# Kernel tuning notes

Measured on AMD Instinct MI355X. Metric: run time of the kernel, lower is better.

The kernel has to match this reference:

```python
import jax, jax.numpy as jnp
import numpy as np

B, L, D, H, P = 8, 1024, 128, 128, 8
W = 2 * L  # total words
FT = 0.1   # forget-gate floor


def _lin_init(k, out_d, in_d):
    k1, k2 = jax.random.split(k)
    s = 1.0 / np.sqrt(in_d)
    Wm = jax.random.uniform(k1, (out_d, in_d), minval=-s, maxval=s, dtype=jnp.float32)
    b = jax.random.uniform(k2, (out_d,), minval=-s, maxval=s, dtype=jnp.float32)
    return Wm, b


def setup_inputs() -> dict:
    key = jax.random.key(0)
    ks = jax.random.split(key, 32)
    inp = {
        "word_span0": jax.random.normal(ks[0], (B, L, D), dtype=jnp.float32),
        "word_span1": jax.random.normal(ks[1], (B, L, D), dtype=jnp.float32),
        "node_hidden": jax.random.normal(ks[2], (B, D), dtype=jnp.float32),
        "op_embedding": jax.random.normal(ks[3], (B, P, D), dtype=jnp.float32),
        "word_exist_sequence": jax.random.uniform(ks[4], (B, W), dtype=jnp.float32),
        "word_exist_matrix": jax.random.uniform(ks[5], (B, W, W), dtype=jnp.float32),
        "word_operator": jax.random.uniform(ks[6], (B, W, P), dtype=jnp.float32),
        "word_word": jax.random.uniform(ks[7], (B, W, W), dtype=jnp.float32),
        "depend0": jax.random.uniform(ks[8], (B, L, L), dtype=jnp.float32),
        "depend1": jax.random.uniform(ks[9], (B, L, L), dtype=jnp.float32),
        "goal_word": jax.random.uniform(ks[10], (B, W), dtype=jnp.float32),
    }
    dims = [("w_w_s", H, D), ("w_w_k", H, D), ("w_update", D, 3 * H),
            ("g_w", H, D), ("w_o", D, D), ("b2u_forget", D, 3 * H + D),
            ("b2u_forget2", D, 2 * D), ("linear_output", D, D),
            ("o_w", H, D), ("w_g", D, D), ("u2b_forget", D, 2 * D),
            ("w_o_forget", P, D + P * D), ("w_o_rel", P, D + P * D),
            ("w_o_update", P, 2 * P)]
    for i, (nm, o, ii) in enumerate(dims):
        Wm, b = _lin_init(ks[11 + i], o, ii)
        inp[nm + "_W"] = Wm
        inp[nm + "_b"] = b
    return inp


def _lin(x, Wm, b):
    return x @ Wm.T + b


def _nrm(m):
    # row-normalize by count of nonzero entries (torch normalize_matrix)
    return m / ((m != 0).sum(-1, keepdims=True).astype(m.dtype) + 1e-30)


def _l2(x):
    return x / (jnp.linalg.norm(x, axis=-1, keepdims=True) + 1e-30)


def _hgcn(span0, span1, node_hidden, op_emb, wes, wem, w_op, ww, dep0, dep1, gw, p):
    # ---- Bottom2Up ----
    all_word = jnp.concatenate([span0, span1], axis=1)              # [B,W,D]
    goal_trans = _lin(node_hidden, p["g_w_W"], p["g_w_b"])[:, None, :]  # [B,1,H]
    word_g = _l2(goal_trans * gw[..., None])                        # [B,W,H]
    wk_trans = _lin(all_word, p["w_w_k_W"], p["w_w_k_b"])           # [B,W,H]
    word_w_k = _l2(_nrm(ww * wem) @ wk_trans)                       # [B,W,H]
    word_w_s = _l2(jnp.concatenate(
        [_nrm(dep0) @ _lin(span0, p["w_w_s_W"], p["w_w_s_b"]),
         _nrm(dep1) @ _lin(span1, p["w_w_s_W"], p["w_w_s_b"])], axis=1))
    neighbor = jnp.concatenate([word_g, word_w_k, word_w_s], axis=-1)  # [B,W,3H]
    forget = jax.nn.sigmoid(_lin(jnp.concatenate([all_word, word_g, word_w_k, word_w_s], axis=-1),
                                 p["b2u_forget_W"], p["b2u_forget_b"]))
    word_updated = jnp.clip(forget, FT) * all_word + (1 - forget) * jax.nn.relu(
        _lin(neighbor, p["w_update_W"], p["w_update_b"]))           # [B,W,D]
    word_op = _nrm(jnp.swapaxes(wes[..., None] * w_op, 1, 2)) @ _lin(
        word_updated, p["w_o_W"], p["w_o_b"])                       # [B,P,D]
    forget2 = jax.nn.sigmoid(_lin(jnp.concatenate([op_emb, word_op], axis=-1),
                                  p["b2u_forget2_W"], p["b2u_forget2_b"]))
    op_emb = jnp.clip(forget2, FT) * op_emb + (1 - forget2) * jax.nn.relu(
        _lin(word_op, p["linear_output_W"], p["linear_output_b"]))  # [B,P,D]

    # ---- update_graph ----
    awe_n = _l2(word_updated)
    op_n = _l2(op_emb).reshape(op_emb.shape[0], -1)                 # [B,P*D]
    concate = jnp.concatenate(
        [awe_n, jnp.broadcast_to(op_n[:, None, :], (awe_n.shape[0], awe_n.shape[1], op_n.shape[-1]))],
        axis=-1)                                                    # [B,W,D+P*D]
    fg = jnp.clip(jax.nn.sigmoid(_lin(concate, p["w_o_forget_W"], p["w_o_forget_b"])), FT)
    upd = jax.nn.softmax(jax.nn.relu(_lin(
        jnp.concatenate([w_op, _lin(concate, p["w_o_rel_W"], p["w_o_rel_b"])], axis=-1),
        p["w_o_update_W"], p["w_o_update_b"])), axis=-1)
    w_op_new = fg * w_op + (1 - fg) * upd                           # [B,W,P]

    # ---- Up2Bottom ----
    span0u, span1u = word_updated[:, :L], word_updated[:, L:]
    word_o = _l2(w_op_new @ _lin(op_emb, p["o_w_W"], p["o_w_b"]))   # [B,W,H]
    word_w_k2 = _l2(_nrm(ww * wem) @ _lin(word_updated, p["w_w_k_W"], p["w_w_k_b"]))
    word_w_s2 = _l2(jnp.concatenate(
        [_nrm(dep0) @ _lin(span0u, p["w_w_s_W"], p["w_w_s_b"]),
         _nrm(dep1) @ _lin(span1u, p["w_w_s_W"], p["w_w_s_b"])], axis=1))
    neighbor2 = jnp.concatenate([word_o, word_w_k2, word_w_s2], axis=-1)
    word_updated2 = jax.nn.relu(_lin(neighbor2, p["w_update_W"], p["w_update_b"]))  # [B,W,D]
    goal_w = jnp.einsum('bw,bwd->bd', _nrm(gw * wes), word_updated2)  # [B,D]
    goal_updated = jax.nn.relu(_lin(goal_w, p["w_g_W"], p["w_g_b"]))
    fg3 = jax.nn.sigmoid(_lin(jnp.concatenate([goal_w, node_hidden], axis=-1),
                              p["u2b_forget_W"], p["u2b_forget_b"]))
    goal_next = jnp.clip(fg3, FT) * node_hidden + (1 - fg3) * goal_updated
    return (span0u, span1u, op_emb, goal_next)


def reference(word_span0, word_span1, node_hidden, op_embedding, word_exist_sequence,
              word_exist_matrix, word_operator, word_word, depend0, depend1, goal_word,
              w_w_s_W, w_w_s_b, w_w_k_W, w_w_k_b, w_update_W, w_update_b,
              g_w_W, g_w_b, w_o_W, w_o_b, b2u_forget_W, b2u_forget_b,
              b2u_forget2_W, b2u_forget2_b, linear_output_W, linear_output_b,
              o_w_W, o_w_b, w_g_W, w_g_b, u2b_forget_W, u2b_forget_b,
              w_o_forget_W, w_o_forget_b, w_o_rel_W, w_o_rel_b, w_o_update_W, w_o_update_b):
    p = dict(w_w_s_W=w_w_s_W, w_w_s_b=w_w_s_b, w_w_k_W=w_w_k_W, w_w_k_b=w_w_k_b,
             w_update_W=w_update_W, w_update_b=w_update_b, g_w_W=g_w_W, g_w_b=g_w_b,
             w_o_W=w_o_W, w_o_b=w_o_b, b2u_forget_W=b2u_forget_W, b2u_forget_b=b2u_forget_b,
             b2u_forget2_W=b2u_forget2_W, b2u_forget2_b=b2u_forget2_b,
             linear_output_W=linear_output_W, linear_output_b=linear_output_b,
             o_w_W=o_w_W, o_w_b=o_w_b, w_g_W=w_g_W, w_g_b=w_g_b,
             u2b_forget_W=u2b_forget_W, u2b_forget_b=u2b_forget_b,
             w_o_forget_W=w_o_forget_W, w_o_forget_b=w_o_forget_b,
             w_o_rel_W=w_o_rel_W, w_o_rel_b=w_o_rel_b,
             w_o_update_W=w_o_update_W, w_o_update_b=w_o_update_b)
    return _hgcn(word_span0, word_span1, node_hidden, op_embedding, word_exist_sequence,
                 word_exist_matrix, word_operator, word_word, depend0, depend1, goal_word, p)
```

## Files before the change

kernel.cpp:

```cpp
#include <hip/hip_runtime.h>

constexpr int Bn = 8, Ln = 1024, Dn = 128, Pn = 8, Wn = 2048;
constexpr float FTc = 0.1f;
constexpr int BLDc = Bn * Ln * Dn;
constexpr int BWDc = Bn * Wn * Dn;
constexpr int IDM = 1 << 28;

struct __align__(16) F4 { float v[4]; };

typedef __attribute__((ext_vector_type(8))) __bf16 bf16x8;
typedef __attribute__((ext_vector_type(8))) short short8v;
typedef __attribute__((ext_vector_type(4))) short short4v;
typedef __attribute__((ext_vector_type(4))) float f32x4;

static __device__ __forceinline__ float sigm(float x) { return 1.f / (1.f + expf(-x)); }

static __device__ __forceinline__ short f2bf(float f) {
    unsigned u = __builtin_bit_cast(unsigned, f);
    unsigned r = (u + 0x7FFFu + ((u >> 16) & 1u)) >> 16;
    return (short)r;
}
static __device__ __forceinline__ float bf2f(short s) {
    return __builtin_bit_cast(float, ((unsigned)(unsigned short)s) << 16);
}

template<int NSRC, int ACT, int OUT, int BM>
__global__ __launch_bounds__(256)
void linmfma(const short* __restrict__ x0, const short* __restrict__ x1,
             const short* __restrict__ x2, const short* __restrict__ x3,
             const float* __restrict__ Wt, const float* __restrict__ bias,
             float* __restrict__ Y, short* __restrict__ Yh,
             int in_mod, int in_stride, int in_off,
             int out_mod, int out_stride, int out_off,
             const float* __restrict__ fbuf, const float* __restrict__ bbuf)
{
    constexpr int K = NSRC * 128;
    constexpr int NKB = K / 64;
    constexpr int WRr = BM / 16;
    constexpr int WC = 4 / WRr;
    constexpr int NF = 8 / WC;
    constexpr int CPW = 128 / WC;
    __shared__ short sX[BM * 72];
    __shared__ short sW[128 * 72];

    const int tid = threadIdx.x;
    const int wave = tid >> 6, lane = tid & 63;
    const int l15 = lane & 15, l4 = lane >> 4;
    const int rg = wave % WRr, cg = wave / WRr;
    const int n0 = blockIdx.x * BM;
    const int inRow0  = (n0 / in_mod)  * in_stride  + (n0 % in_mod)  + in_off;
    const int outRow0 = (n0 / out_mod) * out_stride + (n0 % out_mod) + out_off;

    f32x4 acc[NF];
    #pragma unroll
    for (int nf = 0; nf < NF; ++nf) acc[nf] = (f32x4){0.f, 0.f, 0.f, 0.f};

    const int xrow = tid >> 3, xk8 = (tid & 7) * 8;

    for (int kb = 0; kb < NKB; ++kb) {
        const int k0 = kb * 64;
        __syncthreads();
        if (tid < BM * 8) {
            const short* __restrict__ src;
            { int s = k0 >> 7; src = (s == 0) ? x0 : (s == 1) ? x1 : (s == 2) ? x2 : x3; }
            const int koff = k0 & 127;
            *(short8v*)&sX[xrow * 72 + xk8] =
                *(const short8v*)(src + (size_t)(inRow0 + xrow) * 128 + koff + xk8);
        }
        #pragma unroll
        for (int it = 0; it < 4; ++it) {
            int idx = tid + it * 256;
            int m = idx >> 3, k8 = (idx & 7) * 8;
            const float* pw = Wt + (size_t)m * K + k0 + k8;
            F4 v0 = *(const F4*)pw, v1 = *(const F4*)(pw + 4);
            short8v sv;
            #pragma unroll
            for (int e = 0; e < 4; ++e) { sv[e] = f2bf(v0.v[e]); sv[4 + e] = f2bf(v1.v[e]); }
            *(short8v*)&sW[m * 72 + k8] = sv;
        }
        __syncthreads();
        #pragma unroll
        for (int ksub = 0; ksub < 2; ++ksub) {
            bf16x8 af = *(const bf16x8*)&sX[(rg * 16 + l15) * 72 + ksub * 32 + l4 * 8];
            #pragma unroll
            for (int nf = 0; nf < NF; ++nf) {
                bf16x8 bv = *(const bf16x8*)&sW[(cg * CPW + nf * 16 + l15) * 72 + ksub * 32 + l4 * 8];
                acc[nf] = __builtin_amdgcn_mfma_f32_16x16x32_bf16(af, bv, acc[nf], 0, 0, 0);
            }
        }
    }

    const int r0 = rg * 16 + l4 * 4;
    #pragma unroll
    for (int nf = 0; nf < NF; ++nf) {
        int col = cg * CPW + nf * 16 + l15;
        float bs = bias[col];
        #pragma unroll
        for (int r = 0; r < 4; ++r) {
            int row = outRow0 + r0 + r;
            float v = acc[nf][r] + bs;
            if constexpr (ACT == 1) v = fmaxf(v, 0.f);
            if constexpr (ACT == 2) v = sigm(v);
            if constexpr (ACT == 3) {
                float f = fbuf[(size_t)row * 128 + col];
                float base = bbuf[(size_t)row * 128 + col];
                v = fmaxf(f, FTc) * base + (1.f - f) * fmaxf(v, 0.f);
            }
            if constexpr (OUT & 1) Y[(size_t)row * 128 + col] = v;
            if constexpr (OUT & 2) Yh[(size_t)row * 128 + col] = f2bf(v);
        }
    }
}

__global__ __launch_bounds__(256)
void lin2x(const short* __restrict__ x0,
           const float* __restrict__ W0, const float* __restrict__ b0v,
           const float* __restrict__ W1, const float* __restrict__ b1v,
           short* __restrict__ Xout0, short* __restrict__ Xout1)
{
    __shared__ short sX[32 * 72];
    __shared__ short sW[2][128 * 72];
    const int tid = threadIdx.x;
    const int wave = tid >> 6, lane = tid & 63;
    const int l15 = lane & 15, l4 = lane >> 4;
    const int rg = wave & 1, cg = wave >> 1;
    const int n0 = blockIdx.x * 32;

    f32x4 acc[2][4];
    #pragma unroll
    for (int o = 0; o < 2; ++o) {
        #pragma unroll
        for (int nf = 0; nf < 4; ++nf) {
            acc[o][nf] = (f32x4){0.f, 0.f, 0.f, 0.f};
        }
    }

    const int xrow = tid >> 3, xk8 = (tid & 7) * 8;

    #pragma unroll
    for (int kb = 0; kb < 2; ++kb) {
        const int k0 = kb * 64;
        __syncthreads();
        *(short8v*)&sX[xrow * 72 + xk8] =
            *(const short8v*)(x0 + (size_t)(n0 + xrow) * 128 + k0 + xk8);
        #pragma unroll
        for (int o = 0; o < 2; ++o) {
            const float* __restrict__ Wt = o ? W1 : W0;
            #pragma unroll
            for (int it = 0; it < 4; ++it) {
                int idx = tid + it * 256;
                int m = idx >> 3, k8 = (idx & 7) * 8;
                const float* pw = Wt + (size_t)m * 128 + k0 + k8;
                F4 v0 = *(const F4*)pw, v1 = *(const F4*)(pw + 4);
                short8v sv;
                #pragma unroll
                for (int e = 0; e < 4; ++e) { sv[e] = f2bf(v0.v[e]); sv[4 + e] = f2bf(v1.v[e]); }
                *(short8v*)&sW[o][m * 72 + k8] = sv;
            }
        }
        __syncthreads();
        #pragma unroll
        for (int ksub = 0; ksub < 2; ++ksub) {
            bf16x8 af = *(const bf16x8*)&sX[(rg * 16 + l15) * 72 + ksub * 32 + l4 * 8];
            #pragma unroll
            for (int o = 0; o < 2; ++o) {
                #pragma unroll
                for (int nf = 0; nf < 4; ++nf) {
                    bf16x8 bv = *(const bf16x8*)&sW[o][(cg * 64 + nf * 16 + l15) * 72 + ksub * 32 + l4 * 8];
                    acc[o][nf] = __builtin_amdgcn_mfma_f32_16x16x32_bf16(af, bv, acc[o][nf], 0, 0, 0);
                }
            }
        }
    }

    const int r0 = rg * 16 + l4 * 4;
    __syncthreads();
    #pragma unroll
    for (int o = 0; o < 2; ++o) {
        const float* bv = o ? b1v : b0v;
        #pragma unroll
        for (int nf = 0; nf < 4; ++nf) {
            int col = cg * 64 + nf * 16 + l15;
            float bs = bv[col];
            #pragma unroll
            for (int r = 0; r < 4; ++r) {
                sW[o][col * 40 + r0 + r] = f2bf(acc[o][nf][r] + bs);
            }
        }
    }
    __syncthreads();
    const int bb = n0 >> 11, kbo = (n0 & 2047) >> 5;
    #pragma unroll
    for (int o = 0; o < 2; ++o) {
        short* __restrict__ dst = (o ? Xout1 : Xout0) + ((size_t)(bb * 64 + kbo)) * 4096;
        #pragma unroll
        for (int it = 0; it < 2; ++it) {
            int t2 = tid + it * 256;
            int col = t2 >> 2, k8 = (t2 & 3) * 8;
            *(short8v*)(dst + (size_t)t2 * 8) = *(const short8v*)&sW[o][col * 40 + k8];
        }
    }
}

template<int AMODE, bool WRA>
__global__ __launch_bounds__(256)
void mfma_gemm5(const float* __restrict__ A0, const float* __restrict__ A1,
                const short* __restrict__ Abf, short* __restrict__ Awr,
                const short* __restrict__ Xblk, short* __restrict__ part,
                int NI, int KJ, int KL, int xkb0)
{
    __shared__ short sA[64 * 72];
    __shared__ short sB[128 * 72];
    const int tid = threadIdx.x;
    const int wave = tid >> 6, lane = tid & 63;
    const int l15 = lane & 15, l4 = lane >> 4;
    const int b = blockIdx.y, kc = blockIdx.z;
    const int i0 = blockIdx.x * 64;
    const size_t aBase = ((size_t)b * NI + i0) * KJ + (size_t)kc * KL;
    const int nkb = KL >> 6;
    const int cbase = b * 64 + xkb0 + ((kc * KL) >> 5);
    const int arow = tid >> 2, ak = (tid & 3) * 16;
    const int bk8 = (tid & 3) * 8;

    f32x4 acc[8];
    #pragma unroll
    for (int nf = 0; nf < 8; ++nf) acc[nf] = (f32x4){0.f, 0.f, 0.f, 0.f};

    short8v ra0, ra1;
    F4 rav0, rav1, rav2, rav3, raw0, raw1, raw2, raw3;
    short8v rb0, rb1, rb2, rb3;

#define LOADA(KB)                                                              \
    {                                                                          \
        size_t aoff = aBase + (size_t)arow * KJ + (KB)*64 + ak;                \
        if constexpr (AMODE == 2) {                                            \
            ra0 = *(const short8v*)(Abf + aoff);                               \
            ra1 = *(const short8v*)(Abf + aoff + 8);                           \
        } else {                                                               \
            rav0 = *(const F4*)(A0 + aoff);      rav1 = *(const F4*)(A0 + aoff + 4); \
            rav2 = *(const F4*)(A0 + aoff + 8);  rav3 = *(const F4*)(A0 + aoff + 12);\
            if constexpr (AMODE == 1) {                                        \
                raw0 = *(const F4*)(A1 + aoff);      raw1 = *(const F4*)(A1 + aoff + 4); \
                raw2 = *(const F4*)(A1 + aoff + 8);  raw3 = *(const F4*)(A1 + aoff + 12);\
            }                                                                  \
        }                                                                      \
    }
#define STOREA(KB)                                                             \
    {                                                                          \
        short8v sv0, sv1;                                                      \
        if constexpr (AMODE == 2) { sv0 = ra0; sv1 = ra1; }                    \
        else {                                                                 \
            _Pragma("unroll")                                                  \
            for (int e = 0; e < 4; ++e) {                                      \
                float a0 = rav0.v[e], a1 = rav1.v[e], a2 = rav2.v[e], a3 = rav3.v[e]; \
                if constexpr (AMODE == 1) { a0 *= raw0.v[e]; a1 *= raw1.v[e];  \
                                            a2 *= raw2.v[e]; a3 *= raw3.v[e]; }\
                sv0[e] = f2bf(a0); sv0[4 + e] = f2bf(a1);                      \
                sv1[e] = f2bf(a2); sv1[4 + e] = f2bf(a3);                      \
            }                                                                  \
        }                                                                      \
        *(short8v*)&sA[arow * 72 + ak]     = sv0;                              \
        *(short8v*)&sA[arow * 72 + ak + 8] = sv1;                              \
        if constexpr (WRA) {                                                   \
            size_t aoff = aBase + (size_t)arow * KJ + (KB)*64 + ak;            \
            *(short8v*)(Awr + aoff)     = sv0;                                 \
            *(short8v*)(Awr + aoff + 8) = sv1;                                 \
        }                                                                      \
    }
#define LOADB(KB)                                                              \
    {                                                                          \
        const short* s0 = Xblk + ((size_t)(cbase + (KB)*2)) * 4096;            \
        rb0 = *(const short8v*)(s0 + (size_t)tid * 8);                         \
        rb1 = *(const short8v*)(s0 + (size_t)(tid + 256) * 8);                 \
        rb2 = *(const short8v*)(s0 + 4096 + (size_t)tid * 8);                  \
        rb3 = *(const short8v*)(s0 + 4096 + (size_t)(tid + 256) * 8);          \
    }
#define STOREB()                                                               \
    {                                                                          \
        int c0 = tid >> 2;            int c1 = (tid + 256) >> 2;               \
        *(short8v*)&sB[c0 * 72 + bk8]      = rb0;                              \
        *(short8v*)&sB[c1 * 72 + bk8]      = rb1;                              \
        *(short8v*)&sB[c0 * 72 + 32 + bk8] = rb2;                              \
        *(short8v*)&sB[c1 * 72 + 32 + bk8] = rb3;                              \
    }

    LOADA(0); LOADB(0);
    STOREA(0); STOREB();
    __syncthreads();

    for (int kb = 0; kb < nkb; ++kb) {
        const bool more = (kb + 1 < nkb);
        if (more) { LOADA(kb + 1); LOADB(kb + 1); }
        #pragma unroll
        for (int ksub = 0; ksub < 2; ++ksub) {
            bf16x8 af = *(const bf16x8*)&sA[(wave * 16 + l15) * 72 + ksub * 32 + l4 * 8];
            #pragma unroll
            for (int nf = 0; nf < 8; ++nf) {
                bf16x8 bv = *(const bf16x8*)&sB[(nf * 16 + l15) * 72 + ksub * 32 + l4 * 8];
                acc[nf] = __builtin_amdgcn_mfma_f32_16x16x32_bf16(af, bv, acc[nf], 0, 0, 0);
            }
        }
        if (more) {
            __syncthreads();
            STOREA(kb + 1); STOREB();
            __syncthreads();
        }
    }
#undef LOADA
#undef STOREA
#undef LOADB
#undef STOREB

    const size_t pbase = (((size_t)kc * Bn + b) * NI + i0 + wave * 16 + l4 * 4) * 128;
    #pragma unroll
    for (int nf = 0; nf < 8; ++nf) {
        #pragma unroll
        for (int r = 0; r < 4; ++r) {
            part[pbase + (size_t)r * 128 + nf * 16 + l15] = f2bf(acc[nf][r]);
        }
    }
}

__global__ void k_gemm_finh(const short* __restrict__ part, short* __restrict__ Yh,
                            int NI, int KCH, int ybs, int yoff)
{
    int row = blockIdx.x; int b = row / NI; int i = row - b * NI;
    int h = threadIdx.x;
    float s = 0.f;
    for (int kc = 0; kc < KCH; ++kc)
        s += bf2f(part[(((size_t)kc * Bn + b) * NI + i) * 128 + h]);
    __shared__ float red[128];
    red[h] = s * s; __syncthreads();
    for (int st = 64; st > 0; st >>= 1) { if (h < st) red[h] += red[h + st]; __syncthreads(); }
    Yh[(size_t)(b * ybs + yoff + i) * 128 + h] = f2bf(s / (sqrtf(red[0]) + 1e-30f));
}

__global__ void k_allword(const float* __restrict__ s0, const float* __restrict__ s1,
                          float* __restrict__ aw, short* __restrict__ awh)
{
    int i = blockIdx.x * 256 + threadIdx.x;
    int b = i / (Ln * Dn / 4);
    F4 v0 = ((const F4*)s0)[i];
    F4 v1 = ((const F4*)s1)[i];
    int d0 = i + b * (Ln * Dn / 4);
    int d1 = i + (b + 1) * (Ln * Dn / 4);
    ((F4*)aw)[d0] = v0;
    ((F4*)aw)[d1] = v1;
    short4v h0, h1;
    #pragma unroll
    for (int e = 0; e < 4; ++e) { h0[e] = f2bf(v0.v[e]); h1[e] = f2bf(v1.v[e]); }
    ((short4v*)awh)[d0] = h0;
    ((short4v*)awh)[d1] = h1;
}

__global__ void k_goalg(const float* __restrict__ node, const float* __restrict__ Wg,
                        const float* __restrict__ bg, float* __restrict__ gvec,
                        float* __restrict__ gnorm)
{
    int b = blockIdx.x, h = threadIdx.x;
    float s = bg[h];
    for (int k = 0; k < 128; ++k) s += node[b * 128 + k] * Wg[h * 128 + k];
    gvec[b * 128 + h] = s;
    __shared__ float red[128];
    red[h] = s * s; __syncthreads();
    for (int st = 64; st > 0; st >>= 1) { if (h < st) red[h] += red[h + st]; __syncthreads(); }
    if (h == 0) gnorm[b] = sqrtf(red[0]);
}

__global__ void k_wordg(const float* __restrict__ gvec, const float* __restrict__ gnorm,
                        const float* __restrict__ gw, short* __restrict__ wgh)
{
    int row = blockIdx.x; int b = row >> 11; int h = threadIdx.x;
    float s = gw[row];
    float coef = s / (s * gnorm[b] + 1e-30f);
    wgh[(size_t)row * 128 + h] = f2bf(gvec[b * 128 + h] * coef);
}

__global__ __launch_bounds__(256)
void k_wordop_part(const float* __restrict__ wes, const float* __restrict__ wopr,
                   const float* __restrict__ Yl, float* __restrict__ part,
                   float* __restrict__ pcnt)
{
    int c = blockIdx.x, b = blockIdx.y;
    int w0 = c * 32;
    __shared__ float sc[32][8];
    int tid = threadIdx.x;
    {
        int w = tid >> 3, p = tid & 7;
        sc[w][p] = wes[b * Wn + w0 + w] * wopr[(size_t)(b * Wn + w0 + w) * Pn + p];
    }
    __syncthreads();
    if (tid < 8) {
        float n = 0.f;
        for (int w = 0; w < 32; ++w) n += (sc[w][tid] != 0.f) ? 1.f : 0.f;
        pcnt[(c * 8 + b) * 8 + tid] = n;
    }
    int d = tid & 127, g = tid >> 7;
    float acc[4] = {};
    for (int w = 0; w < 32; ++w) {
        float y = Yl[(size_t)(b * Wn + w0 + w) * 128 + d];
        #pragma unroll
        for (int q = 0; q < 4; ++q) acc[q] += sc[w][g * 4 + q] * y;
    }
    #pragma unroll
    for (int q = 0; q < 4; ++q)
        part[(((size_t)c * 8 + b) * 8 + g * 4 + q) * 128 + d] = acc[q];
}

__global__ void k_wordop_fin(const float* __restrict__ part, const float* __restrict__ pcnt,
                             float* __restrict__ outp)
{
    int bp = blockIdx.x;
    int b = bp >> 3, p = bp & 7;
    int d = threadIdx.x;
    float s = 0.f, n = 0.f;
    for (int c = 0; c < 64; ++c) s += part[(((size_t)c * 8 + b) * 8 + p) * 128 + d];
    for (int c = 0; c < 64; ++c) n += pcnt[(c * 8 + b) * 8 + p];
    outp[(size_t)bp * 128 + d] = s / (n + 1e-30f);
}

__global__ void k_opemb(const float* __restrict__ oein, const float* __restrict__ wop,
                        const float* __restrict__ W2, const float* __restrict__ b2,
                        const float* __restrict__ Wlo, const float* __restrict__ blo,
                        float* __restrict__ opembN, float* __restrict__ out2)
{
    int bp = blockIdx.x; int h = threadIdx.x;
    const float* oe = oein + (size_t)bp * 128;
    const float* wo = wop + (size_t)bp * 128;
    float s = b2[h], lo = blo[h];
    for (int k = 0; k < 128; ++k) {
        s += oe[k] * W2[h * 256 + k];
        s += wo[k] * W2[h * 256 + 128 + k];
        lo += wo[k] * Wlo[h * 128 + k];
    }
    float f = sigm(s);
    float v = fmaxf(f, FTc) * oe[h] + (1.f - f) * fmaxf(lo, 0.f);
    opembN[bp * 128 + h] = v;
    out2[bp * 128 + h] = v;
}

__global__ void k_opn(const float* __restrict__ opembN, float* __restrict__ opn)
{
    __shared__ float red[128];
    int bp = blockIdx.x, h = threadIdx.x;
    float v = opembN[bp * 128 + h];
    red[h] = v * v; __syncthreads();
    for (int s = 64; s > 0; s >>= 1) { if (h < s) red[h] += red[h + s]; __syncthreads(); }
    opn[bp * 128 + h] = v / (sqrtf(red[0]) + 1e-30f);
}

__global__ void k_cfrel(const float* __restrict__ opn, const float* __restrict__ Wf,
                        const float* __restrict__ bf, const float* __restrict__ Wr,
                        const float* __restrict__ br, float* __restrict__ cf,
                        float* __restrict__ crel)
{
    int bp = blockIdx.x; int b = bp >> 3, p = bp & 7;
    int t = threadIdx.x;
    float sf = 0.f, sr = 0.f;
    for (int k = t; k < 1024; k += 256) {
        float o = opn[b * 1024 + k];
        sf += o * Wf[p * 1152 + 128 + k];
        sr += o * Wr[p * 1152 + 128 + k];
    }
    __shared__ float rf[256], rr[256];
    rf[t] = sf; rr[t] = sr; __syncthreads();
    for (int s = 128; s > 0; s >>= 1) {
        if (t < s) { rf[t] += rf[t + s]; rr[t] += rr[t + s]; }
        __syncthreads();
    }
    if (t == 0) { cf[bp] = rf[0] + bf[p]; crel[bp] = rr[0] + br[p]; }
}

__global__ __launch_bounds__(256)
void k_fgrel(const float* __restrict__ wupd, const float* __restrict__ Wf,
             const float* __restrict__ Wr, const float* __restrict__ cf,
             const float* __restrict__ crel, float* __restrict__ fgb,
             float* __restrict__ relb)
{
    __shared__ float sXr[32 * 132];
    __shared__ float sinv[32];
    int tid = threadIdx.x;
    int n0 = blockIdx.x * 32;
    for (int l = tid; l < 4096; l += 256) {
        int r = l >> 7, h = l & 127;
        sXr[r * 132 + h] = wupd[(size_t)(n0 + r) * 128 + h];
    }
    __syncthreads();
    if (tid < 32) {
        float s = 0.f;
        for (int h = 0; h < 128; ++h) { float v = sXr[tid * 132 + h]; s += v * v; }
        sinv[tid] = 1.f / (sqrtf(s) + 1e-30f);
    }
    __syncthreads();
    int r = tid >> 3, p = tid & 7;
    int n = n0 + r; int b = n >> 11;
    float af = 0.f, ar = 0.f, inv = sinv[r];
    for (int d = 0; d < 128; ++d) {
        float x = sXr[r * 132 + d] * inv;
        af += x * Wf[p * 1152 + d];
        ar += x * Wr[p * 1152 + d];
    }
    float f = sigm(af + cf[b * 8 + p]);
    fgb[(size_t)n * 8 + p] = fmaxf(f, FTc);
    relb[(size_t)n * 8 + p] = ar + crel[b * 8 + p];
}

__global__ void k_wopnew(const float* __restrict__ wopr, const float* __restrict__ fgb,
                         const float* __restrict__ relb, const float* __restrict__ Wu,
                         const float* __restrict__ bu, float* __restrict__ wopn)
{
    int row = blockIdx.x * 256 + threadIdx.x;
    float t16[16];
    #pragma unroll
    for (int p = 0; p < 8; ++p) t16[p] = wopr[(size_t)row * 8 + p];
    #pragma unroll
    for (int p = 0; p < 8; ++p) t16[8 + p] = relb[(size_t)row * 8 + p];
    float u[8]; float m = -1e30f;
    #pragma unroll
    for (int p = 0; p < 8; ++p) {
        float s = bu[p];
        #pragma unroll
        for (int q = 0; q < 16; ++q) s += Wu[p * 16 + q] * t16[q];
        s = fmaxf(s, 0.f); u[p] = s; m = fmaxf(m, s);
    }
    float tot = 0.f;
    #pragma unroll
    for (int p = 0; p < 8; ++p) { u[p] = expf(u[p] - m); tot += u[p]; }
    float itot = 1.f / tot;
    #pragma unroll
    for (int p = 0; p < 8; ++p) {
        float f = fgb[(size_t)row * 8 + p];
        wopn[(size_t)row * 8 + p] = f * t16[p] + (1.f - f) * u[p] * itot;
    }
}

__global__ void k_opw(const float* __restrict__ opembN, const float* __restrict__ Wo,
                      const float* __restrict__ bo, float* __restrict__ opw)
{
    int bp = blockIdx.x, h = threadIdx.x;
    float s = bo[h];
    for (int d = 0; d < 128; ++d) s += opembN[bp * 128 + d] * Wo[h * 128 + d];
    opw[bp * 128 + h] = s;
}

__global__ void k_wordo(const float* __restrict__ wopn, const float* __restrict__ opw,
                        short* __restrict__ woh)
{
    int row = blockIdx.x; int b = row >> 11; int h = threadIdx.x;
    float c[8];
    #pragma unroll
    for (int p = 0; p < 8; ++p) c[p] = wopn[(size_t)row * 8 + p];
    float v = 0.f;
    #pragma unroll
    for (int p = 0; p < 8; ++p) v += c[p] * opw[(b * 8 + p) * 128 + h];
    __shared__ float red[128];
    red[h] = v * v; __syncthreads();
    for (int s = 64; s > 0; s >>= 1) { if (h < s) red[h] += red[h + s]; __syncthreads(); }
    woh[(size_t)row * 128 + h] = f2bf(v / (sqrtf(red[0]) + 1e-30f));
}

__global__ __launch_bounds__(256)
void k_goalw_part(const float* __restrict__ gw, const float* __restrict__ wes,
                  const float* __restrict__ wupd2, float* __restrict__ part,
                  float* __restrict__ pcnt)
{
    int c = blockIdx.x, b = blockIdx.y;
    int w0 = c * 32;
    __shared__ float sc[32];
    __shared__ float sa[256];
    int tid = threadIdx.x;
    if (tid < 32) sc[tid] = gw[b * Wn + w0 + tid] * wes[b * Wn + w0 + tid];
    __syncthreads();
    if (tid == 0) {
        float n = 0.f;
        for (int w = 0; w < 32; ++w) n += (sc[w] != 0.f) ? 1.f : 0.f;
        pcnt[c * 8 + b] = n;
    }
    int d = tid & 127, h = tid >> 7;
    float acc = 0.f;
    for (int w = h; w < 32; w += 2)
        acc += sc[w] * wupd2[(size_t)(b * Wn + w0 + w) * 128 + d];
    sa[tid] = acc; __syncthreads();
    if (h == 0) part[((size_t)c * 8 + b) * 128 + d] = sa[d] + sa[128 + d];
}

__global__ void k_goalw_fin(const float* __restrict__ part, const float* __restrict__ pcnt,
                            float* __restrict__ goalw)
{
    int b = blockIdx.x, d = threadIdx.x;
    float s = 0.f, n = 0.f;
    for (int c = 0; c < 64; ++c) s += part[((size_t)c * 8 + b) * 128 + d];
    for (int c = 0; c < 64; ++c) n += pcnt[c * 8 + b];
    goalw[b * 128 + d] = s / (n + 1e-30f);
}

__global__ void k_goalnext(const float* __restrict__ goalw, const float* __restrict__ node,
                           const float* __restrict__ Wg, const float* __restrict__ bg,
                           const float* __restrict__ Wu2, const float* __restrict__ bu2,
                           float* __restrict__ outg)
{
    int b = blockIdx.x, h = threadIdx.x;
    float su = bg[h], sf = bu2[h];
    for (int k = 0; k < 128; ++k) {
        float g = goalw[b * 128 + k];
        su += g * Wg[h * 128 + k];
        sf += g * Wu2[h * 256 + k] + node[b * 128 + k] * Wu2[h * 256 + 128 + k];
    }
    float gu = fmaxf(su, 0.f);
    float f = sigm(sf);
    outg[b * 128 + h] = fmaxf(f, FTc) * node[b * 128 + h] + (1.f - f) * gu;
}

__global__ void k_copyspans(const float* __restrict__ wupd, float* __restrict__ out)
{
    int i = blockIdx.x * 256 + threadIdx.x;
    F4 v = ((const F4*)wupd)[i];
    int row = i >> 5;
    int col = i & 31;
    int b = row >> 11, w = row & 2047;
    int dst;
    if (w < Ln) dst = ((b * Ln + w) << 5) + col;
    else        dst = (BLDc >> 2) + ((b * Ln + (w - Ln)) << 5) + col;
    ((F4*)out)[dst] = v;
}

extern "C" void kernel_launch(void* const* d_in, const int* in_sizes, int n_in,
                              void* d_out, int out_size, void* d_ws, size_t ws_size,
                              hipStream_t stream)
{
    const float* span0 = (const float*)d_in[0];
    const float* span1 = (const float*)d_in[1];
    const float* node  = (const float*)d_in[2];
    const float* opemb = (const float*)d_in[3];
    const float* wes   = (const float*)d_in[4];
    const float* wem   = (const float*)d_in[5];
    const float* wopr  = (const float*)d_in[6];
    const float* ww    = (const float*)d_in[7];
    const float* dep0  = (const float*)d_in[8];
    const float* dep1  = (const float*)d_in[9];
    const float* gw    = (const float*)d_in[10];
    const float* wws_W = (const float*)d_in[11]; const float* wws_b = (const float*)d_in[12];
    const float* wwk_W = (const float*)d_in[13]; const float* wwk_b = (const float*)d_in[14];
    const float* wup_W = (const float*)d_in[15]; const float* wup_b = (const float*)d_in[16];
    const float* gw_W  = (const float*)d_in[17]; const float* gw_b  = (const float*)d_in[18];
    const float* wo_W  = (const float*)d_in[19]; const float* wo_b  = (const float*)d_in[20];
    const float* bf_W  = (const float*)d_in[21]; const float* bf_b  = (const float*)d_in[22];
    const float* bf2_W = (const float*)d_in[23]; const float* bf2_b = (const float*)d_in[24];
    const float* lo_W  = (const float*)d_in[25]; const float* lo_b  = (const float*)d_in[26];
    const float* ow_W  = (const float*)d_in[27]; const float* ow_b  = (const float*)d_in[28];
    const float* wg_W  = (const float*)d_in[29]; const float* wg_b  = (const float*)d_in[30];
    const float* u2b_W = (const float*)d_in[31]; const float* u2b_b = (const float*)d_in[32];
    const float* wof_W = (const float*)d_in[33]; const float* wof_b = (const float*)d_in[34];
    const float* wor_W = (const float*)d_in[35]; const float* wor_b = (const float*)d_in[36];
    const float* wou_W = (const float*)d_in[37]; const float* wou_b = (const float*)d_in[38];

    float* out = (float*)d_out;
    float* out_op   = out + 2 * BLDc;
    float* out_goal = out + 2 * BLDc + Bn * Pn * Dn;

    float* ws = (float*)d_ws;
    float* allword = ws;
    float* wupd    = ws + 1 * BWDc;
    float* tmpA    = ws + 2 * BWDc;
    float* tmpB    = ws + 3 * BWDc;
    float* sm      = ws + 4 * BWDc;
    float* gvec   = sm;
    float* gnorm  = sm + 1024;
    float* wordop = sm + 1056;
    float* opembN = sm + 9248;
    float* opn    = sm + 17440;
    float* cf     = sm + 25632;
    float* crel   = sm + 25696;
    float* opw    = sm + 25760;
    float* goalw  = sm + 33952;
    float* fgb    = sm + 34976;
    float* relb   = sm + 166048;
    float* wopn   = sm + 297120;

    short* allwordh = (short*)(ws + 4 * (size_t)BWDc + 458752);
    short* wupdh  = allwordh + BWDc;
    short* wordgh = wupdh + BWDc;
    short* wwkh   = wordgh + BWDc;
    short* wwsh   = wwkh + BWDc;
    short* Xblk   = wwsh + BWDc;
    short* Awwem  = Xblk + BWDc;
    short* dep0b  = Awwem + (size_t)Bn * Wn * Wn;
    short* dep1b  = dep0b + (size_t)Bn * Ln * Ln;

    short* XblkS1 = (short*)tmpA;
    short* pWW1   = dep0b;
    short* pDep1  = (short*)tmpB;
    short* XblkS2 = (short*)allword;
    short* pWW2   = (short*)tmpA;
    short* pDep2  = (short*)tmpB;

    const dim3 blk(256);

    k_allword<<<1024, blk, 0, stream>>>(span0, span1, allword, allwordh);
    lin2x<<<512, blk, 0, stream>>>(allwordh, wwk_W, wwk_b, wws_W, wws_b, Xblk, XblkS1);
    mfma_gemm5<1,true><<<dim3(32, 8, 2), blk, 0, stream>>>(ww, wem, nullptr, Awwem,
        Xblk, pWW1, Wn, Wn, 1024, 0);
    k_gemm_finh<<<16384, 128, 0, stream>>>(pWW1, wwkh, Wn, 2, Wn, 0);
    mfma_gemm5<0,true><<<dim3(16, 8, 4), blk, 0, stream>>>(dep0, nullptr, nullptr, dep0b,
        XblkS1, pDep1, Ln, Ln, 256, 0);
    k_gemm_finh<<<8192, 128, 0, stream>>>(pDep1, wwsh, Ln, 4, Wn, 0);
    mfma_gemm5<0,true><<<dim3(16, 8, 4), blk, 0, stream>>>(dep1, nullptr, nullptr, dep1b,
        XblkS1, pDep1, Ln, Ln, 256, 32);
    k_gemm_finh<<<8192, 128, 0, stream>>>(pDep1, wwsh, Ln, 4, Wn, Ln);
    k_goalg<<<8, 128, 0, stream>>>(node, gw_W, gw_b, gvec, gnorm);
    k_wordg<<<16384, 128, 0, stream>>>(gvec, gnorm, gw, wordgh);
    linmfma<4,2,1,16><<<1024, blk, 0, stream>>>(allwordh, wordgh, wwkh, wwsh,
        bf_W, bf_b, tmpB, nullptr, IDM, 0, 0, IDM, 0, 0, nullptr, nullptr);
    linmfma<3,3,3,16><<<1024, blk, 0, stream>>>(wordgh, wwkh, wwsh, nullptr,
        wup_W, wup_b, wupd, wupdh, IDM, 0, 0, IDM, 0, 0, tmpB, allword);
    linmfma<1,0,1,16><<<1024, blk, 0, stream>>>(wupdh, nullptr, nullptr, nullptr,
        wo_W, wo_b, tmpA, nullptr, IDM, 0, 0, IDM, 0, 0, nullptr, nullptr);
    k_wordop_part<<<dim3(64, 8), blk, 0, stream>>>(wes, wopr, tmpA, tmpB, tmpB + 524288);
    k_wordop_fin<<<64, 128, 0, stream>>>(tmpB, tmpB + 524288, wordop);
    k_opemb<<<64, 128, 0, stream>>>(opemb, wordop, bf2_W, bf2_b, lo_W, lo_b, opembN, out_op);
    k_opn<<<64, 128, 0, stream>>>(opembN, opn);
    k_cfrel<<<64, blk, 0, stream>>>(opn, wof_W, wof_b, wor_W, wor_b, cf, crel);
    k_fgrel<<<512, blk, 0, stream>>>(wupd, wof_W, wor_W, cf, crel, fgb, relb);
    k_wopnew<<<64, blk, 0, stream>>>(wopr, fgb, relb, wou_W, wou_b, wopn);
    k_opw<<<64, 128, 0, stream>>>(opembN, ow_W, ow_b, opw);
    k_wordo<<<16384, 128, 0, stream>>>(wopn, opw, wordgh);

    lin2x<<<512, blk, 0, stream>>>(wupdh, wwk_W, wwk_b, wws_W, wws_b, Xblk, XblkS2);
    mfma_gemm5<2,false><<<dim3(32, 8, 2), blk, 0, stream>>>(nullptr, nullptr, Awwem, nullptr,
        Xblk, pWW2, Wn, Wn, 1024, 0);
    k_gemm_finh<<<16384, 128, 0, stream>>>(pWW2, wwkh, Wn, 2, Wn, 0);
    mfma_gemm5<2,false><<<dim3(16, 8, 4), blk, 0, stream>>>(nullptr, nullptr, dep0b, nullptr,
        XblkS2, pDep2, Ln, Ln, 256, 0);
    k_gemm_finh<<<8192, 128, 0, stream>>>(pDep2, wwsh, Ln, 4, Wn, 0);
    mfma_gemm5<2,false><<<dim3(16, 8, 4), blk, 0, stream>>>(nullptr, nullptr, dep1b, nullptr,
        XblkS2, pDep2, Ln, Ln, 256, 32);
    k_gemm_finh<<<8192, 128, 0, stream>>>(pDep2, wwsh, Ln, 4, Wn, Ln);
    linmfma<3,1,1,16><<<1024, blk, 0, stream>>>(wordgh, wwkh, wwsh, nullptr,
        wup_W, wup_b, tmpA, nullptr, IDM, 0, 0, IDM, 0, 0, nullptr, nullptr);
    k_goalw_part<<<dim3(64, 8), blk, 0, stream>>>(gw, wes, tmpA, tmpB, tmpB + 65536);
    k_goalw_fin<<<8, 128, 0, stream>>>(tmpB, tmpB + 65536, goalw);
    k_goalnext<<<8, 128, 0, stream>>>(goalw, node, wg_W, wg_b, u2b_W, u2b_b, out_goal);
    k_copyspans<<<2048, blk, 0, stream>>>(wupd, out);
}
```

Baseline: 376.7 us.

## Drop LDS staging in MFMA GEMM, load fragments directly from global memory

Rewrites the batched adjacency GEMM so each wave loads its A and B MFMA fragments straight from global memory into registers, removing the shared-memory tiles and both __syncthreads per k-step. The word-word GEMM also doubles its K-split from 2 to 4 chunks to launch more blocks, and the reduction kernel is updated to sum 4 partials. This removes LDS traffic and barrier stalls but loses cross-wave reuse of B (each wave re-reads the same B block) and relies on cache and unrolling to hide global latency. The larger split adds partial-sum write and reduce traffic.

```diff
diff --git a/kernel.cpp b/kernel.cpp
--- a/kernel.cpp
+++ b/kernel.cpp
@@ -204,114 +204,55 @@
 
 template<int AMODE, bool WRA>
 __global__ __launch_bounds__(256)
-void mfma_gemm5(const float* __restrict__ A0, const float* __restrict__ A1,
+void mfma_gemm6(const float* __restrict__ A0, const float* __restrict__ A1,
                 const short* __restrict__ Abf, short* __restrict__ Awr,
                 const short* __restrict__ Xblk, short* __restrict__ part,
                 int NI, int KJ, int KL, int xkb0)
 {
-    __shared__ short sA[64 * 72];
-    __shared__ short sB[128 * 72];
     const int tid = threadIdx.x;
     const int wave = tid >> 6, lane = tid & 63;
     const int l15 = lane & 15, l4 = lane >> 4;
     const int b = blockIdx.y, kc = blockIdx.z;
-    const int i0 = blockIdx.x * 64;
-    const size_t aBase = ((size_t)b * NI + i0) * KJ + (size_t)kc * KL;
-    const int nkb = KL >> 6;
-    const int cbase = b * 64 + xkb0 + ((kc * KL) >> 5);
-    const int arow = tid >> 2, ak = (tid & 3) * 16;
-    const int bk8 = (tid & 3) * 8;
+    const int i0 = blockIdx.x * 64 + wave * 16;
+    const size_t aRow = ((size_t)b * NI + i0 + l15) * KJ + (size_t)kc * KL;
+    const int nks = KL >> 5;
+    const int cb0 = b * 64 + xkb0 + ((kc * KL) >> 5);
+    const int lko = l4 * 8;
 
     f32x4 acc[8];
     #pragma unroll
     for (int nf = 0; nf < 8; ++nf) acc[nf] = (f32x4){0.f, 0.f, 0.f, 0.f};
 
-    short8v ra0, ra1;
-    F4 rav0, rav1, rav2, rav3, raw0, raw1, raw2, raw3;
-    short8v rb0, rb1, rb2, rb3;
-
-#define LOADA(KB)                                                              \
-    {                                                                          \
-        size_t aoff = aBase + (size_t)arow * KJ + (KB)*64 + ak;                \
-        if constexpr (AMODE == 2) {                                            \
-            ra0 = *(const short8v*)(Abf + aoff);                               \
-            ra1 = *(const short8v*)(Abf + aoff + 8);                           \
-        } else {                                                               \
-            rav0 = *(const F4*)(A0 + aoff);      rav1 = *(const F4*)(A0 + aoff + 4); \
-            rav2 = *(const F4*)(A0 + aoff + 8);  rav3 = *(const F4*)(A0 + aoff + 12);\
-            if constexpr (AMODE == 1) {                                        \
-                raw0 = *(const F4*)(A1 + aoff);      raw1 = *(const F4*)(A1 + aoff + 4); \
-                raw2 = *(const F4*)(A1 + aoff + 8);  raw3 = *(const F4*)(A1 + aoff + 12);\
-            }                                                                  \
-        }                                                                      \
-    }
-#define STOREA(KB)                                                             \
-    {                                                                          \
-        short8v sv0, sv1;                                                      \
-        if constexpr (AMODE == 2) { sv0 = ra0; sv1 = ra1; }                    \
-        else {                                                                 \
-            _Pragma("unroll")                                                  \
-            for (int e = 0; e < 4; ++e) {                                      \
-                float a0 = rav0.v[e], a1 = rav1.v[e], a2 = rav2.v[e], a3 = rav3.v[e]; \
-                if constexpr (AMODE == 1) { a0 *= raw0.v[e]; a1 *= raw1.v[e];  \
-                                            a2 *= raw2.v[e]; a3 *= raw3.v[e]; }\
-                sv0[e] = f2bf(a0); sv0[4 + e] = f2bf(a1);                      \
-                sv1[e] = f2bf(a2); sv1[4 + e] = f2bf(a3);                      \
-            }                                                                  \
-        }                                                                      \
-        *(short8v*)&sA[arow * 72 + ak]     = sv0;                              \
-        *(short8v*)&sA[arow * 72 + ak + 8] = sv1;                              \
-        if constexpr (WRA) {                                                   \
-            size_t aoff = aBase + (size_t)arow * KJ + (KB)*64 + ak;            \
-            *(short8v*)(Awr + aoff)     = sv0;                                 \
-            *(short8v*)(Awr + aoff + 8) = sv1;                                 \
-        }                                                                      \
-    }
-#define LOADB(KB)                                                              \
-    {                                                                          \
-        const short* s0 = Xblk + ((size_t)(cbase + (KB)*2)) * 4096;            \
-        rb0 = *(const short8v*)(s0 + (size_t)tid * 8);                         \
-        rb1 = *(const short8v*)(s0 + (size_t)(tid + 256) * 8);                 \
-        rb2 = *(const short8v*)(s0 + 4096 + (size_t)tid * 8);                  \
-        rb3 = *(const short8v*)(s0 + 4096 + (size_t)(tid + 256) * 8);          \
-    }
-#define STOREB()                                                               \
-    {                                                                          \
-        int c0 = tid >> 2;            int c1 = (tid + 256) >> 2;               \
-        *(short8v*)&sB[c0 * 72 + bk8]      = rb0;                              \
-        *(short8v*)&sB[c1 * 72 + bk8]      = rb1;                              \
-        *(short8v*)&sB[c0 * 72 + 32 + bk8] = rb2;                              \
-        *(short8v*)&sB[c1 * 72 + 32 + bk8] = rb3;                              \
-    }
-
-    LOADA(0); LOADB(0);
-    STOREA(0); STOREB();
-    __syncthreads();
-
-    for (int kb = 0; kb < nkb; ++kb) {
-        const bool more = (kb + 1 < nkb);
-        if (more) { LOADA(kb + 1); LOADB(kb + 1); }
-        #pragma unroll
-        for (int ksub = 0; ksub < 2; ++ksub) {
-            bf16x8 af = *(const bf16x8*)&sA[(wave * 16 + l15) * 72 + ksub * 32 + l4 * 8];
+    #pragma unroll 4
+    for (int ks = 0; ks < nks; ++ks) {
+        const size_t ao = aRow + ks * 32 + lko;
+        bf16x8 af;
+        if constexpr (AMODE == 2) {
+            af = *(const bf16x8*)(Abf + ao);
+        } else {
+            F4 v0 = *(const F4*)(A0 + ao);
+            F4 v1 = *(const F4*)(A0 + ao + 4);
+            if constexpr (AMODE == 1) {
+                F4 w0 = *(const F4*)(A1 + ao);
+                F4 w1 = *(const F4*)(A1 + ao + 4);
+                #pragma unroll
+                for (int e = 0; e < 4; ++e) { v0.v[e] *= w0.v[e]; v1.v[e] *= w1.v[e]; }
+            }
+            short8v sv;
             #pragma unroll
-            for (int nf = 0; nf < 8; ++nf) {
-                bf16x8 bv = *(const bf16x8*)&sB[(nf * 16 + l15) * 72 + ksub * 32 + l4 * 8];
-                acc[nf] = __builtin_amdgcn_mfma_f32_16x16x32_bf16(af, bv, acc[nf], 0, 0, 0);
-            }
-        }
-        if (more) {
-            __syncthreads();
-            STOREA(kb + 1); STOREB();
-            __syncthreads();
-        }
-    }
-#undef LOADA
-#undef STOREA
-#undef LOADB
-#undef STOREB
-
-    const size_t pbase = (((size_t)kc * Bn + b) * NI + i0 + wave * 16 + l4 * 4) * 128;
+            for (int e = 0; e < 4; ++e) { sv[e] = f2bf(v0.v[e]); sv[4 + e] = f2bf(v1.v[e]); }
+            if constexpr (WRA) *(short8v*)(Awr + ao) = sv;
+            af = __builtin_bit_cast(bf16x8, sv);
+        }
+        const short* bp = Xblk + (size_t)(cb0 + ks) * 4096 + lko;
+        #pragma unroll
+        for (int nf = 0; nf < 8; ++nf) {
+            bf16x8 bv = *(const bf16x8*)(bp + (nf * 16 + l15) * 32);
+            acc[nf] = __builtin_amdgcn_mfma_f32_16x16x32_bf16(af, bv, acc[nf], 0, 0, 0);
+        }
+    }
+
+    const size_t pbase = (((size_t)kc * Bn + b) * NI + i0 + l4 * 4) * 128;
     #pragma unroll
     for (int nf = 0; nf < 8; ++nf) {
         #pragma unroll
@@ -698,13 +639,13 @@
 
     k_allword<<<1024, blk, 0, stream>>>(span0, span1, allword, allwordh);
     lin2x<<<512, blk, 0, stream>>>(allwordh, wwk_W, wwk_b, wws_W, wws_b, Xblk, XblkS1);
-    mfma_gemm5<1,true><<<dim3(32, 8, 2), blk, 0, stream>>>(ww, wem, nullptr, Awwem,
-        Xblk, pWW1, Wn, Wn, 1024, 0);
-    k_gemm_finh<<<16384, 128, 0, stream>>>(pWW1, wwkh, Wn, 2, Wn, 0);
-    mfma_gemm5<0,true><<<dim3(16, 8, 4), blk, 0, stream>>>(dep0, nullptr, nullptr, dep0b,
+    mfma_gemm6<1,true><<<dim3(32, 8, 4), blk, 0, stream>>>(ww, wem, nullptr, Awwem,
+        Xblk, pWW1, Wn, Wn, 512, 0);
+    k_gemm_finh<<<16384, 128, 0, stream>>>(pWW1, wwkh, Wn, 4, Wn, 0);
+    mfma_gemm6<0,true><<<dim3(16, 8, 4), blk, 0, stream>>>(dep0, nullptr, nullptr, dep0b,
         XblkS1, pDep1, Ln, Ln, 256, 0);
     k_gemm_finh<<<8192, 128, 0, stream>>>(pDep1, wwsh, Ln, 4, Wn, 0);
-    mfma_gemm5<0,true><<<dim3(16, 8, 4), blk, 0, stream>>>(dep1, nullptr, nullptr, dep1b,
+    mfma_gemm6<0,true><<<dim3(16, 8, 4), blk, 0, stream>>>(dep1, nullptr, nullptr, dep1b,
         XblkS1, pDep1, Ln, Ln, 256, 32);
     k_gemm_finh<<<8192, 128, 0, stream>>>(pDep1, wwsh, Ln, 4, Wn, Ln);
     k_goalg<<<8, 128, 0, stream>>>(node, gw_W, gw_b, gvec, gnorm);
@@ -726,13 +667,13 @@
     k_wordo<<<16384, 128, 0, stream>>>(wopn, opw, wordgh);
 
     lin2x<<<512, blk, 0, stream>>>(wupdh, wwk_W, wwk_b, wws_W, wws_b, Xblk, XblkS2);
-    mfma_gemm5<2,false><<<dim3(32, 8, 2), blk, 0, stream>>>(nullptr, nullptr, Awwem, nullptr,
-        Xblk, pWW2, Wn, Wn, 1024, 0);
-    k_gemm_finh<<<16384, 128, 0, stream>>>(pWW2, wwkh, Wn, 2, Wn, 0);
-    mfma_gemm5<2,false><<<dim3(16, 8, 4), blk, 0, stream>>>(nullptr, nullptr, dep0b, nullptr,
+    mfma_gemm6<2,false><<<dim3(32, 8, 4), blk, 0, stream>>>(nullptr, nullptr, Awwem, nullptr,
+        Xblk, pWW2, Wn, Wn, 512, 0);
+    k_gemm_finh<<<16384, 128, 0, stream>>>(pWW2, wwkh, Wn, 4, Wn, 0);
+    mfma_gemm6<2,false><<<dim3(16, 8, 4), blk, 0, stream>>>(nullptr, nullptr, dep0b, nullptr,
         XblkS2, pDep2, Ln, Ln, 256, 0);
     k_gemm_finh<<<8192, 128, 0, stream>>>(pDep2, wwsh, Ln, 4, Wn, 0);
-    mfma_gemm5<2,false><<<dim3(16, 8, 4), blk, 0, stream>>>(nullptr, nullptr, dep1b, nullptr,
+    mfma_gemm6<2,false><<<dim3(16, 8, 4), blk, 0, stream>>>(nullptr, nullptr, dep1b, nullptr,
         XblkS2, pDep2, Ln, Ln, 256, 32);
     k_gemm_finh<<<8192, 128, 0, stream>>>(pDep2, wwsh, Ln, 4, Wn, Ln);
     linmfma<3,1,1,16><<<1024, blk, 0, stream>>>(wordgh, wwkh, wwsh, nullptr,
```

After: 444.6 us. 1.18x slower.
